# Optimization experiments

Hardware: AMD Instinct MI355X
Metric: run time of the kernel (lower is better)

Reference implementation:

```python
import jax, jax.numpy as jnp
import numpy as np

N = 20000       # nodes
E = 100000      # edges
STEPS = 4
ND = 128        # node feature dim
ED = 128        # edge feature dim
NIN = 128       # node input dim
EIN = 291       # edge input dim (2 + 17*17)
H = 64          # mpn edge-mlp hidden


def _lin(x, w, b):
    return x @ w + b


def setup_inputs():
    key = jax.random.key(0)
    ks = jax.random.split(key, 16)

    def w(k, i, o):
        return (jax.random.normal(k, (i, o), jnp.float32) / np.float32(np.sqrt(i)))

    d = {}
    d["x"] = jax.random.normal(ks[0], (N, NIN), jnp.float32)
    d["edge_attr"] = jax.random.normal(ks[1], (E, EIN), jnp.float32)
    d["edge_index"] = jax.random.randint(ks[2], (2, E), 0, N, jnp.int32)
    # node embedding MLP: NIN -> 128 -> ND (ReLU between, none after last)
    d["new0"] = w(ks[3], NIN, 128); d["neb0"] = jnp.zeros(128, jnp.float32)
    d["new1"] = w(ks[4], 128, ND); d["neb1"] = jnp.zeros(ND, jnp.float32)
    # edge embedding MLP: EIN -> 64 -> ED
    d["eew0"] = w(ks[5], EIN, 64); d["eeb0"] = jnp.zeros(64, jnp.float32)
    d["eew1"] = w(ks[6], 64, ED); d["eeb1"] = jnp.zeros(ED, jnp.float32)
    # MPN edge MLP (skip=True): 2*(2*ND) + 2*ED = 768 -> 64 -> ED, ReLU after each
    d["mew0"] = w(ks[7], 4 * ND + 2 * ED, H); d["meb0"] = jnp.zeros(H, jnp.float32)
    d["mew1"] = w(ks[8], H, ED); d["meb1"] = jnp.zeros(ED, jnp.float32)
    # MPN node MLP: 2*ND + ED = 384 -> ND, ReLU
    d["mnw0"] = w(ks[9], 2 * ND + ED, ND); d["mnb0"] = jnp.zeros(ND, jnp.float32)
    # classification MLP: ED -> 64 -> 32 -> 1
    d["cw0"] = w(ks[10], ED, 64); d["cb0"] = jnp.zeros(64, jnp.float32)
    d["cw1"] = w(ks[11], 64, 32); d["cb1"] = jnp.zeros(32, jnp.float32)
    d["cw2"] = w(ks[12], 32, 1); d["cb2"] = jnp.zeros(1, jnp.float32)
    return d


def reference(x, edge_attr, edge_index,
              new0, neb0, new1, neb1,
              eew0, eeb0, eew1, eeb1,
              mew0, meb0, mew1, meb1,
              mnw0, mnb0,
              cw0, cb0, cw1, cb1, cw2, cb2):
    relu = jax.nn.relu
    j, i = edge_index[0], edge_index[1]  # j: source, i: target

    nf = _lin(relu(_lin(x, new0, neb0)), new1, neb1)          # [N, ND]
    ef = _lin(relu(_lin(edge_attr, eew0, eeb0)), eew1, eeb1)  # [E, ED]
    nf0, ef0 = nf, ef

    for _ in range(STEPS):
        # skip connections: concat initial features
        nfc = jnp.concatenate([nf0, nf], axis=1)  # [N, 2*ND]
        efc = jnp.concatenate([ef0, ef], axis=1)  # [E, 2*ED]
        x_i = nfc[i]  # [E, 2*ND] target
        x_j = nfc[j]  # [E, 2*ND] source
        # edge update MLP (ReLU after both layers)
        h = relu(_lin(jnp.concatenate([x_i, x_j, efc], axis=1), mew0, meb0))
        ef = relu(_lin(h, mew1, meb1))  # [E, ED]
        # message: mlp_node([x_i, edge_attr_new]) aggregated at target i
        msg = relu(_lin(jnp.concatenate([x_i, ef], axis=1), mnw0, mnb0))  # [E, ND]
        nf = jax.ops.segment_sum(msg, i, num_segments=N)  # [N, ND]

    out = relu(_lin(ef, cw0, cb0))
    out = relu(_lin(out, cw1, cb1))
    out = _lin(out, cw2, cb2)  # [E, 1]
    return out
```

## Files before the change

### kernel.cpp

```cpp
#include <hip/hip_runtime.h>
#include <hip/hip_bf16.h>

#define ND 128
#define ED 128
#define NIN 128
#define EIN 291
#define KPAD 320
#define HH 64
#define TM 32
#define TS 64
#define GSE 768
#define MAXGE 3

typedef __attribute__((ext_vector_type(8))) short short8;
typedef __attribute__((ext_vector_type(4))) float float4_;

__device__ __forceinline__ unsigned short f2bf(float f)
{
    union { float f; unsigned u; } v; v.f = f;
    unsigned u = v.u;
    unsigned r = (u + 0x7FFFu + ((u >> 16) & 1u)) >> 16;
    return (unsigned short)r;
}
__device__ __forceinline__ float bf2f(unsigned short s)
{
    union { unsigned u; float f; } v; v.u = ((unsigned)s) << 16;
    return v.f;
}

template<int T, int KC, int K>
__device__ __forceinline__ void stage_frags(const unsigned short* __restrict__ src,
                                            unsigned short* __restrict__ wreg,
                                            int t, int k0)
{
    constexpr int TOT = T * KC * 64;
#pragma unroll
    for (int it = 0; it < TOT / 256; it++) {
        int idx = it * 256 + t;
        int f = idx >> 6, l = idx & 63;
        int col = (f / KC) * 16 + (l & 15);
        int k = (f % KC) * 32 + ((l >> 4) * 8);
        *(short8*)&wreg[idx * 8] = *(const short8*)&src[(size_t)col * K + k0 + k];
    }
}
#define FRAG(wreg, f, lane) (*(const short8*)&(wreg)[(((f) << 6) + (lane)) * 8])

__global__ __launch_bounds__(256) void zero_k(float* __restrict__ p, int n4)
{
    int idx = blockIdx.x * 256 + threadIdx.x;
    if (idx < n4) ((float4*)p)[idx] = make_float4(0.f, 0.f, 0.f, 0.f);
}

__global__ __launch_bounds__(256) void hist_k(const int* __restrict__ tgti,
                                              int* __restrict__ deg, int E)
{
    int e = blockIdx.x * 256 + threadIdx.x;
    if (e < E) atomicAdd(&deg[tgti[e]], 1);
}

__global__ __launch_bounds__(256) void scan_k(const int* __restrict__ deg,
                                              int* __restrict__ row_ptr,
                                              int* __restrict__ cursor, int N, int E)
{
    __shared__ int part[256];
    const int t = threadIdx.x;
    const int chunk = (N + 255) / 256;
    const int base = t * chunk;
    int s = 0;
    for (int k = 0; k < chunk; k++) { int idx = base + k; if (idx < N) s += deg[idx]; }
    part[t] = s;
    __syncthreads();
    for (int off = 1; off < 256; off <<= 1) {
        int v = (t >= off) ? part[t - off] : 0;
        __syncthreads();
        part[t] += v;
        __syncthreads();
    }
    int run = (t == 0) ? 0 : part[t - 1];
    for (int k = 0; k < chunk; k++) {
        int idx = base + k;
        if (idx < N) { row_ptr[idx] = run; cursor[idx] = run; run += deg[idx]; }
    }
    if (t == 255) row_ptr[N] = E;
}

__global__ __launch_bounds__(256) void scatter_k(const int* __restrict__ tgti,
                                                 int* __restrict__ cursor,
                                                 int* __restrict__ csr_eid, int E)
{
    int e = blockIdx.x * 256 + threadIdx.x;
    if (e < E) {
        int p = atomicAdd(&cursor[tgti[e]], 1);
        csr_eid[p] = e;
    }
}

__global__ __launch_bounds__(256) void agg_k(const int* __restrict__ row_ptr,
                                             const int* __restrict__ csr_eid,
                                             const unsigned short* __restrict__ msg,
                                             unsigned short* __restrict__ nf_bf, int N)
{
    int n = blockIdx.x * 2 + (threadIdx.x >> 7);
    int c = threadIdx.x & 127;
    if (n >= N) return;
    int beg = row_ptr[n], end = row_ptr[n + 1];
    float acc = 0.f;
    for (int k = beg; k < end; k++) {
        int e = csr_eid[k];
        acc += bf2f(msg[(size_t)e * ND + c]);
    }
    nf_bf[(size_t)n * ND + c] = f2bf(acc);
}

__global__ __launch_bounds__(256) void wprep_k(
    const float* __restrict__ mew0, const float* __restrict__ mew1, const float* __restrict__ mnw0,
    const float* __restrict__ eew0, const float* __restrict__ eew1, const float* __restrict__ cw0,
    const float* __restrict__ new0, const float* __restrict__ new1,
    unsigned short* __restrict__ w0T, unsigned short* __restrict__ w1T,
    unsigned short* __restrict__ wmT, unsigned short* __restrict__ w0eT,
    unsigned short* __restrict__ w1eT, unsigned short* __restrict__ cw0T,
    unsigned short* __restrict__ w0nT, unsigned short* __restrict__ w1nT)
{
    int idx = blockIdx.x * 256 + threadIdx.x;
    if (idx < 49152) {
        int c = idx / 768, k = idx % 768;
        w0T[idx] = f2bf(mew0[k * 64 + c]);
    } else if (idx < 57344) {
        int j = idx - 49152; int c = j / 64, k = j % 64;
        w1T[j] = f2bf(mew1[k * 128 + c]);
    } else if (idx < 106496) {
        int j = idx - 57344; int c = j / 384, k = j % 384;
        wmT[j] = f2bf(mnw0[k * 128 + c]);
    } else if (idx < 126976) {
        int j = idx - 106496; int c = j / KPAD, k = j % KPAD;
        w0eT[j] = (k < EIN) ? f2bf(eew0[k * 64 + c]) : (unsigned short)0;
    } else if (idx < 135168) {
        int j = idx - 126976; int c = j / 64, k = j % 64;
        w1eT[j] = f2bf(eew1[k * 128 + c]);
    } else if (idx < 143360) {
        int j = idx - 135168; int c = j / 128, k = j % 128;
        cw0T[j] = f2bf(cw0[k * 64 + c]);
    } else if (idx < 159744) {
        int j = idx - 143360; int c = j / 128, k = j % 128;
        w0nT[j] = f2bf(new0[k * 128 + c]);
    } else if (idx < 176128) {
        int j = idx - 159744; int c = j / 128, k = j % 128;
        w1nT[j] = f2bf(new1[k * 128 + c]);
    }
}

__global__ __launch_bounds__(256) void node_embed_k(
    const float* __restrict__ x,
    const unsigned short* __restrict__ w0nT, const float* __restrict__ b0,
    const unsigned short* __restrict__ w1nT, const float* __restrict__ b1,
    unsigned short* __restrict__ nf0_bf, unsigned short* __restrict__ nf_bf, int N)
{
    const int t = threadIdx.x;
    const int n0 = blockIdx.x * TM;
    __shared__ unsigned short wreg[8192];
    __shared__ unsigned short xin[TM][130];
    __shared__ unsigned short h_bf[TM][130];

#pragma unroll
    for (int it = 0; it < 4; it++) {
        int idx = it * 256 + t;
        int r = idx >> 5, c4 = idx & 31;
        int node = n0 + r; if (node >= N) node = N - 1;
        float4 v = *(const float4*)(x + (size_t)node * NIN + c4 * 4);
        unsigned lo = (unsigned)f2bf(v.x) | ((unsigned)f2bf(v.y) << 16);
        unsigned hi = (unsigned)f2bf(v.z) | ((unsigned)f2bf(v.w) << 16);
        *(uint2*)&xin[r][c4 * 4] = make_uint2(lo, hi);
    }

    const int w = t >> 6, lane = t & 63, quad = lane >> 4, n16 = lane & 15;
    const int m = w & 1, nh = w >> 1;

    float4_ acc[4];
#pragma unroll
    for (int q = 0; q < 4; q++) acc[q] = (float4_){0.f, 0.f, 0.f, 0.f};
#pragma unroll
    for (int hf = 0; hf < 2; hf++) {
        stage_frags<8, 2, 128>(w0nT, wreg, t, hf * 64);
        __syncthreads();
#pragma unroll
        for (int kc = 0; kc < 2; kc++) {
            short8 a = *(const short8*)&xin[m * 16 + n16][hf * 64 + kc * 32 + quad * 8];
#pragma unroll
            for (int tt = 0; tt < 4; tt++) {
                short8 b = FRAG(wreg, (nh * 4 + tt) * 2 + kc, lane);
                acc[tt] = __builtin_amdgcn_mfma_f32_16x16x32_bf16(a, b, acc[tt], 0, 0, 0);
            }
        }
        __syncthreads();
    }
#pragma unroll
    for (int tt = 0; tt < 4; tt++) {
        int c = nh * 64 + tt * 16 + n16;
        float bias = b0[c];
#pragma unroll
        for (int r4 = 0; r4 < 4; r4++)
            h_bf[m * 16 + quad * 4 + r4][c] = f2bf(fmaxf(acc[tt][r4] + bias, 0.f));
    }
    __syncthreads();

    float4_ acc2[4];
#pragma unroll
    for (int q = 0; q < 4; q++) acc2[q] = (float4_){0.f, 0.f, 0.f, 0.f};
#pragma unroll
    for (int hf = 0; hf < 2; hf++) {
        stage_frags<8, 2, 128>(w1nT, wreg, t, hf * 64);
        __syncthreads();
#pragma unroll
        for (int kc = 0; kc < 2; kc++) {
            short8 a = *(const short8*)&h_bf[m * 16 + n16][hf * 64 + kc * 32 + quad * 8];
#pragma unroll
            for (int tt = 0; tt < 4; tt++) {
                short8 b = FRAG(wreg, (nh * 4 + tt) * 2 + kc, lane);
                acc2[tt] = __builtin_amdgcn_mfma_f32_16x16x32_bf16(a, b, acc2[tt], 0, 0, 0);
            }
        }
        __syncthreads();
    }
#pragma unroll
    for (int tt = 0; tt < 4; tt++) {
        int c = nh * 64 + tt * 16 + n16;
        float bias = b1[c];
#pragma unroll
        for (int r4 = 0; r4 < 4; r4++) {
            int row = m * 16 + quad * 4 + r4;
            int node = n0 + row;
            if (node < N) {
                unsigned short v = f2bf(acc2[tt][r4] + bias);
                nf0_bf[(size_t)node * ND + c] = v;
                nf_bf[(size_t)node * ND + c] = v;
            }
        }
    }
}

__global__ __launch_bounds__(256, 3) void edge_embed_k(
    const float* __restrict__ ea,
    const unsigned short* __restrict__ w0eT, const float* __restrict__ b0,
    const unsigned short* __restrict__ w1eT, const float* __restrict__ b1,
    unsigned short* __restrict__ ef0_bf, unsigned short* __restrict__ ef_bf,
    int E, int ntiles)
{
    const int t = threadIdx.x;
    __shared__ unsigned short w0reg[10240];
    __shared__ unsigned short w1reg[8192];
    __shared__ unsigned short hsl[4][16 * 66];

    const int w = t >> 6, lane = t & 63, quad = lane >> 4, n16 = lane & 15;

    stage_frags<8, 2, 64>(w1eT, w1reg, t, 0);

    int ng = 0;
    int tile[MAXGE];
#pragma unroll
    for (int g = 0; g < MAXGE; g++) {
        int tl = blockIdx.x + g * GSE;
        if (tl < ntiles) { tile[g] = tl; ng = g + 1; }
        else tile[g] = 0;
    }

    float4_ accL[MAXGE][4];
#pragma unroll
    for (int g = 0; g < MAXGE; g++)
#pragma unroll
        for (int q = 0; q < 4; q++) accL[g][q] = (float4_){0.f, 0.f, 0.f, 0.f};

#pragma unroll
    for (int hf = 0; hf < 2; hf++) {
        __syncthreads();
        stage_frags<4, 5, KPAD>(w0eT, w0reg, t, hf * 160);
        __syncthreads();
#pragma unroll
        for (int g = 0; g < MAXGE; g++) {
            if (g < ng) {
                int e = tile[g] * 64 + w * 16 + n16; if (e >= E) e = E - 1;
                const float* src = ea + (size_t)e * EIN;
#pragma unroll
                for (int kc = 0; kc < 5; kc++) {
                    int k = hf * 160 + kc * 32 + quad * 8;
                    union { short8 s; uint4 u; } av;
                    if (k + 8 <= EIN) {
                        float4 v0 = *(const float4*)(src + k);
                        float4 v1 = *(const float4*)(src + k + 4);
                        av.u.x = (unsigned)f2bf(v0.x) | ((unsigned)f2bf(v0.y) << 16);
                        av.u.y = (unsigned)f2bf(v0.z) | ((unsigned)f2bf(v0.w) << 16);
                        av.u.z = (unsigned)f2bf(v1.x) | ((unsigned)f2bf(v1.y) << 16);
                        av.u.w = (unsigned)f2bf(v1.z) | ((unsigned)f2bf(v1.w) << 16);
                    } else {
                        unsigned short vv[8];
#pragma unroll
                        for (int j = 0; j < 8; j++)
                            vv[j] = (k + j < EIN) ? f2bf(src[k + j]) : (unsigned short)0;
                        av.u.x = (unsigned)vv[0] | ((unsigned)vv[1] << 16);
                        av.u.y = (unsigned)vv[2] | ((unsigned)vv[3] << 16);
                        av.u.z = (unsigned)vv[4] | ((unsigned)vv[5] << 16);
                        av.u.w = (unsigned)vv[6] | ((unsigned)vv[7] << 16);
                    }
#pragma unroll
                    for (int tt = 0; tt < 4; tt++) {
                        short8 b = FRAG(w0reg, tt * 5 + kc, lane);
                        accL[g][tt] = __builtin_amdgcn_mfma_f32_16x16x32_bf16(av.s, b, accL[g][tt], 0, 0, 0);
                    }
                }
            }
        }
    }

#pragma unroll
    for (int g = 0; g < MAXGE; g++) {
        if (g < ng) {
#pragma unroll
            for (int tt = 0; tt < 4; tt++) {
                int c = tt * 16 + n16;
                float bias = b0[c];
#pragma unroll
                for (int r4 = 0; r4 < 4; r4++)
                    hsl[w][(quad * 4 + r4) * 66 + c] = f2bf(fmaxf(accL[g][tt][r4] + bias, 0.f));
            }
            float4_ acc2[8];
#pragma unroll
            for (int q = 0; q < 8; q++) acc2[q] = (float4_){0.f, 0.f, 0.f, 0.f};
#pragma unroll
            for (int kc = 0; kc < 2; kc++) {
                short8 a2 = *(const short8*)&hsl[w][n16 * 66 + kc * 32 + quad * 8];
#pragma unroll
                for (int tt = 0; tt < 8; tt++)
                    acc2[tt] = __builtin_amdgcn_mfma_f32_16x16x32_bf16(
                        a2, FRAG(w1reg, tt * 2 + kc, lane), acc2[tt], 0, 0, 0);
            }
#pragma unroll
            for (int tt = 0; tt < 8; tt++) {
                int c = tt * 16 + n16;
                float bias = b1[c];
#pragma unroll
                for (int r4 = 0; r4 < 4; r4++) {
                    int e = tile[g] * 64 + w * 16 + quad * 4 + r4;
                    if (e < E) {
                        unsigned short v = f2bf(acc2[tt][r4] + bias);
                        ef0_bf[(size_t)e * ED + c] = v;
                        ef_bf[(size_t)e * ED + c] = v;
                    }
                }
            }
        }
    }
}

__global__ __launch_bounds__(256, 3) void edge_step_k(
    const int* __restrict__ srcj, const int* __restrict__ tgti,
    const unsigned short* __restrict__ nf0_bf, const unsigned short* __restrict__ nf_bf,
    const unsigned short* __restrict__ ef0_bf, unsigned short* __restrict__ ef_bf,
    unsigned short* __restrict__ msg,
    const unsigned short* __restrict__ w0T, const float* __restrict__ meb0,
    const unsigned short* __restrict__ w1T, const float* __restrict__ meb1,
    const unsigned short* __restrict__ wmT, const float* __restrict__ mnb0,
    int E, int wmsg)
{
    const int t = threadIdx.x;
    const int e0 = blockIdx.x * TS;
    __shared__ unsigned short wreg[16384];
    __shared__ unsigned short hef[4][2080];

    const int w = t >> 6, lane = t & 63, quad = lane >> 4, n16 = lane & 15;
    int ec = e0 + w * 16 + n16; if (ec >= E) ec = E - 1;
    const int ti = tgti[ec], sj = srcj[ec];

    const unsigned short* pAs[6] = {
        nf0_bf + (size_t)ti * ND + quad * 8,
        nf_bf  + (size_t)ti * ND + quad * 8,
        nf0_bf + (size_t)sj * ND + quad * 8,
        nf_bf  + (size_t)sj * ND + quad * 8,
        ef0_bf + (size_t)ec * ED + quad * 8,
        ef_bf  + (size_t)ec * ED + quad * 8 };

    float4_ accL[4];
#pragma unroll
    for (int q = 0; q < 4; q++) accL[q] = (float4_){0.f, 0.f, 0.f, 0.f};
#pragma unroll
    for (int hf = 0; hf < 3; hf++) {
        short8 a8[8];
#pragma unroll
        for (int q2 = 0; q2 < 8; q2++)
            a8[q2] = *(const short8*)(pAs[hf * 2 + (q2 >> 2)] + (q2 & 3) * 32);
        stage_frags<4, 8, 768>(w0T, wreg, t, hf * 256);
        __syncthreads();
#pragma unroll
        for (int kc = 0; kc < 8; kc++) {
#pragma unroll
            for (int tt = 0; tt < 4; tt++) {
                short8 b = FRAG(wreg, tt * 8 + kc, lane);
                accL[tt] = __builtin_amdgcn_mfma_f32_16x16x32_bf16(a8[kc], b, accL[tt], 0, 0, 0);
            }
        }
        __syncthreads();
    }

#pragma unroll
    for (int tt = 0; tt < 4; tt++) {
        int c = tt * 16 + n16;
        float bias = meb0[c];
#pragma unroll
        for (int r4 = 0; r4 < 4; r4++)
            hef[w][(quad * 4 + r4) * 66 + c] = f2bf(fmaxf(accL[tt][r4] + bias, 0.f));
    }

    stage_frags<8, 2, 64>(w1T, wreg, t, 0);
    __syncthreads();
    {
        float4_ acc[8];
#pragma unroll
        for (int q = 0; q < 8; q++) acc[q] = (float4_){0.f, 0.f, 0.f, 0.f};
#pragma unroll
        for (int kc = 0; kc < 2; kc++) {
            short8 a = *(const short8*)&hef[w][n16 * 66 + kc * 32 + quad * 8];
#pragma unroll
            for (int tt = 0; tt < 8; tt++) {
                short8 b = FRAG(wreg, tt * 2 + kc, lane);
                acc[tt] = __builtin_amdgcn_mfma_f32_16x16x32_bf16(a, b, acc[tt], 0, 0, 0);
            }
        }
#pragma unroll
        for (int tt = 0; tt < 8; tt++) {
            int c = tt * 16 + n16;
            float bias = meb1[c];
#pragma unroll
            for (int r4 = 0; r4 < 4; r4++) {
                int row = quad * 4 + r4;
                unsigned short v = f2bf(fmaxf(acc[tt][r4] + bias, 0.f));
                hef[w][row * 130 + c] = v;
                int e = e0 + w * 16 + row;
                if (e < E) ef_bf[(size_t)e * ED + c] = v;
            }
        }
    }
    __syncthreads();

    if (wmsg) {
        float4_ accM[8];
#pragma unroll
        for (int q = 0; q < 8; q++) accM[q] = (float4_){0.f, 0.f, 0.f, 0.f};
#pragma unroll
        for (int j = 0; j < 3; j++) {
            short8 a4[4];
            if (j < 2) {
#pragma unroll
                for (int q2 = 0; q2 < 4; q2++)
                    a4[q2] = *(const short8*)(pAs[j] + q2 * 32);
            } else {
#pragma unroll
                for (int q2 = 0; q2 < 4; q2++)
                    a4[q2] = *(const short8*)&hef[w][n16 * 130 + q2 * 32 + quad * 8];
            }
            stage_frags<8, 4, 384>(wmT, wreg, t, j * 128);
            __syncthreads();
#pragma unroll
            for (int kc = 0; kc < 4; kc++) {
#pragma unroll
                for (int tt = 0; tt < 8; tt++) {
                    short8 b = FRAG(wreg, tt * 4 + kc, lane);
                    accM[tt] = __builtin_amdgcn_mfma_f32_16x16x32_bf16(a4[kc], b, accM[tt], 0, 0, 0);
                }
            }
            __syncthreads();
        }
#pragma unroll
        for (int tt = 0; tt < 8; tt++) {
            int c = tt * 16 + n16;
            float bias = mnb0[c];
#pragma unroll
            for (int r4 = 0; r4 < 4; r4++) {
                int row = w * 16 + quad * 4 + r4;
                int e = e0 + row;
                if (e < E)
                    msg[(size_t)e * ND + c] = f2bf(fmaxf(accM[tt][r4] + bias, 0.f));
            }
        }
    }
}

__global__ __launch_bounds__(256) void classify_k(
    const unsigned short* __restrict__ ef_bf,
    const unsigned short* __restrict__ cw0T, const float* __restrict__ cb0,
    const float* __restrict__ cw1, const float* __restrict__ cb1,
    const float* __restrict__ cw2, const float* __restrict__ cb2,
    float* __restrict__ out, int E)
{
    const int t = threadIdx.x;
    const int e0 = blockIdx.x * TM;
    __shared__ unsigned short h0_bf[TM][66];
    __shared__ float h1[TM][33];

    const int w = t >> 6, lane = t & 63, quad = lane >> 4, n16 = lane & 15;
    const int m = w & 1;
    const int erow = m * 16 + n16;
    int ec = e0 + erow; if (ec >= E) ec = E - 1;
    const unsigned short* pa = ef_bf + (size_t)ec * ED + quad * 8;

    {
        const int cb = (w >> 1) * 32;
        float4_ acc0 = {0.f, 0.f, 0.f, 0.f}, acc1 = acc0;
        const unsigned short* b0p = cw0T + (size_t)(cb + n16) * 128 + quad * 8;
        const unsigned short* b1p = b0p + (size_t)16 * 128;
#pragma unroll
        for (int kc = 0; kc < 4; kc++) {
            short8 a  = *(const short8*)(pa + kc * 32);
            short8 bb0 = *(const short8*)(b0p + kc * 32);
            short8 bb1 = *(const short8*)(b1p + kc * 32);
            acc0 = __builtin_amdgcn_mfma_f32_16x16x32_bf16(a, bb0, acc0, 0, 0, 0);
            acc1 = __builtin_amdgcn_mfma_f32_16x16x32_bf16(a, bb1, acc1, 0, 0, 0);
        }
#pragma unroll
        for (int t2 = 0; t2 < 2; t2++) {
            int c = cb + t2 * 16 + n16;
            float bias = cb0[c];
            float4_ ac = t2 ? acc1 : acc0;
#pragma unroll
            for (int r4 = 0; r4 < 4; r4++)
                h0_bf[m * 16 + quad * 4 + r4][c] = f2bf(fmaxf(ac[r4] + bias, 0.f));
        }
    }
    __syncthreads();

    {
        int c = t & 31;
        int rbase = (t >> 5) * 4;
#pragma unroll
        for (int q = 0; q < 4; q++) {
            int r = rbase + q;
            float acc = cb1[c];
#pragma unroll 8
            for (int k = 0; k < 64; k++) acc += bf2f(h0_bf[r][k]) * cw1[k * 32 + c];
            h1[r][c] = fmaxf(acc, 0.f);
        }
    }
    __syncthreads();

    if (t < TM) {
        int e = e0 + t;
        if (e < E) {
            float a = cb2[0];
#pragma unroll
            for (int k = 0; k < 32; k++) a += h1[t][k] * cw2[k];
            out[e] = a;
        }
    }
}

extern "C" void kernel_launch(void* const* d_in, const int* in_sizes, int n_in,
                              void* d_out, int out_size, void* d_ws, size_t ws_size,
                              hipStream_t stream)
{
    const float* x    = (const float*)d_in[0];
    const float* ea   = (const float*)d_in[1];
    const int*   eidx = (const int*)d_in[2];
    const float* new0 = (const float*)d_in[3];  const float* neb0 = (const float*)d_in[4];
    const float* new1 = (const float*)d_in[5];  const float* neb1 = (const float*)d_in[6];
    const float* eew0 = (const float*)d_in[7];  const float* eeb0 = (const float*)d_in[8];
    const float* eew1 = (const float*)d_in[9];  const float* eeb1 = (const float*)d_in[10];
    const float* mew0 = (const float*)d_in[11]; const float* meb0 = (const float*)d_in[12];
    const float* mew1 = (const float*)d_in[13]; const float* meb1 = (const float*)d_in[14];
    const float* mnw0 = (const float*)d_in[15]; const float* mnb0 = (const float*)d_in[16];
    const float* cw0  = (const float*)d_in[17]; const float* cb0  = (const float*)d_in[18];
    const float* cw1  = (const float*)d_in[19]; const float* cb1  = (const float*)d_in[20];
    const float* cw2  = (const float*)d_in[21]; const float* cb2  = (const float*)d_in[22];

    const int N = in_sizes[0] / NIN;
    const int E = in_sizes[2] / 2;
    const int* srcj = eidx;
    const int* tgti = eidx + E;

    char* wsb = (char*)d_ws;
    unsigned short* nf0_bf = (unsigned short*)wsb;
    unsigned short* nf_bf  = nf0_bf + (size_t)N * ND;
    unsigned short* ef0_bf = nf_bf + (size_t)N * ND;
    unsigned short* ef_bf  = ef0_bf + (size_t)E * ED;
    unsigned short* msg    = ef_bf + (size_t)E * ED;
    unsigned short* w0T  = msg + (size_t)E * ND;
    unsigned short* w1T  = w0T + 49152;
    unsigned short* wmT  = w1T + 8192;
    unsigned short* w0eT = wmT + 49152;
    unsigned short* w1eT = w0eT + 64 * KPAD;
    unsigned short* cw0T = w1eT + 8192;
    unsigned short* w0nT = cw0T + 8192;
    unsigned short* w1nT = w0nT + 16384;
    int* deg     = (int*)(w1nT + 16384);
    int* cursor  = deg + N;
    int* row_ptr = cursor + N;
    int* csr_eid = row_ptr + (N + 4);

    const int eblocks32 = (E + TM - 1) / TM;
    const int nblocks32 = (N + TM - 1) / TM;
    const int ntiles64 = (E + 63) / 64;

    wprep_k<<<(176128 + 255) / 256, 256, 0, stream>>>(mew0, mew1, mnw0, eew0, eew1, cw0,
                                                      new0, new1,
                                                      w0T, w1T, wmT, w0eT, w1eT, cw0T,
                                                      w0nT, w1nT);

    zero_k<<<((2 * N) / 4 + 255) / 256, 256, 0, stream>>>((float*)deg, (2 * N) / 4);
    hist_k<<<(E + 255) / 256, 256, 0, stream>>>(tgti, deg, E);
    scan_k<<<1, 256, 0, stream>>>(deg, row_ptr, cursor, N, E);
    scatter_k<<<(E + 255) / 256, 256, 0, stream>>>(tgti, cursor, csr_eid, E);

    node_embed_k<<<nblocks32, 256, 0, stream>>>(x, w0nT, neb0, w1nT, neb1,
                                                nf0_bf, nf_bf, N);
    edge_embed_k<<<GSE, 256, 0, stream>>>(ea, w0eT, eeb0, w1eT, eeb1,
                                          ef0_bf, ef_bf, E, ntiles64);

    for (int s = 0; s < 4; s++) {
        edge_step_k<<<ntiles64, 256, 0, stream>>>(srcj, tgti, nf0_bf, nf_bf,
                                                  ef0_bf, ef_bf, msg,
                                                  w0T, meb0, w1T, meb1, wmT, mnb0,
                                                  E, (s < 3) ? 1 : 0);
        if (s < 3)
            agg_k<<<(N + 1) / 2, 256, 0, stream>>>(row_ptr, csr_eid, msg, nf_bf, N);
    }

    classify_k<<<eblocks32, 256, 0, stream>>>(ef_bf, cw0T, cb0, cw1, cb1, cw2, cb2,
                                              (float*)d_out, E);
}
```

Measured before the change: 760.1 us.

## Load MFMA weight fragments directly from global in pre-swizzled layout, drop LDS staging

The weight-prep kernel now writes the edge-step weights already arranged in MFMA B-fragment order. The edge-step kernel reads each fragment straight from global memory (mostly L2-resident) instead of copying it into a 32KB LDS buffer with block barriers. Removing that buffer and the barriers cuts LDS use, and launch bounds rise to 4 blocks per CU for more occupancy. The cost is many more redundant global/L2 loads of weights per wave and possible register pressure under the tighter bound.

```diff
diff --git a/kernel.cpp b/kernel.cpp
--- a/kernel.cpp
+++ b/kernel.cpp
@@ -44,6 +44,7 @@
     }
 }
 #define FRAG(wreg, f, lane) (*(const short8*)&(wreg)[(((f) << 6) + (lane)) * 8])
+#define GFRAG(wp, f, lane) (*(const short8*)&(wp)[(((f) << 6) + (lane)) * 8])
 
 __global__ __launch_bounds__(256) void zero_k(float* __restrict__ p, int n4)
 {
@@ -116,21 +117,29 @@
     const float* __restrict__ mew0, const float* __restrict__ mew1, const float* __restrict__ mnw0,
     const float* __restrict__ eew0, const float* __restrict__ eew1, const float* __restrict__ cw0,
     const float* __restrict__ new0, const float* __restrict__ new1,
-    unsigned short* __restrict__ w0T, unsigned short* __restrict__ w1T,
-    unsigned short* __restrict__ wmT, unsigned short* __restrict__ w0eT,
+    unsigned short* __restrict__ w0F, unsigned short* __restrict__ w1F,
+    unsigned short* __restrict__ wmF, unsigned short* __restrict__ w0eT,
     unsigned short* __restrict__ w1eT, unsigned short* __restrict__ cw0T,
     unsigned short* __restrict__ w0nT, unsigned short* __restrict__ w1nT)
 {
     int idx = blockIdx.x * 256 + threadIdx.x;
     if (idx < 49152) {
-        int c = idx / 768, k = idx % 768;
-        w0T[idx] = f2bf(mew0[k * 64 + c]);
+        int j = idx & 7, l = (idx >> 3) & 63, f = idx >> 9;
+        int col = (f / 24) * 16 + (l & 15);
+        int k = (f % 24) * 32 + ((l >> 4) * 8) + j;
+        w0F[idx] = f2bf(mew0[k * 64 + col]);
     } else if (idx < 57344) {
-        int j = idx - 49152; int c = j / 64, k = j % 64;
-        w1T[j] = f2bf(mew1[k * 128 + c]);
+        int i2 = idx - 49152;
+        int j = i2 & 7, l = (i2 >> 3) & 63, f = i2 >> 9;
+        int col = (f / 2) * 16 + (l & 15);
+        int k = (f % 2) * 32 + ((l >> 4) * 8) + j;
+        w1F[i2] = f2bf(mew1[k * 128 + col]);
     } else if (idx < 106496) {
-        int j = idx - 57344; int c = j / 384, k = j % 384;
-        wmT[j] = f2bf(mnw0[k * 128 + c]);
+        int i2 = idx - 57344;
+        int j = i2 & 7, l = (i2 >> 3) & 63, f = i2 >> 9;
+        int col = (f / 12) * 16 + (l & 15);
+        int k = (f % 12) * 32 + ((l >> 4) * 8) + j;
+        wmF[i2] = f2bf(mnw0[k * 128 + col]);
     } else if (idx < 126976) {
         int j = idx - 106496; int c = j / KPAD, k = j % KPAD;
         w0eT[j] = (k < EIN) ? f2bf(eew0[k * 64 + c]) : (unsigned short)0;
@@ -350,26 +359,25 @@
     }
 }
 
-__global__ __launch_bounds__(256, 3) void edge_step_k(
+__global__ __launch_bounds__(256, 4) void edge_step_k(
     const int* __restrict__ srcj, const int* __restrict__ tgti,
     const unsigned short* __restrict__ nf0_bf, const unsigned short* __restrict__ nf_bf,
     const unsigned short* __restrict__ ef0_bf, unsigned short* __restrict__ ef_bf,
     unsigned short* __restrict__ msg,
-    const unsigned short* __restrict__ w0T, const float* __restrict__ meb0,
-    const unsigned short* __restrict__ w1T, const float* __restrict__ meb1,
-    const unsigned short* __restrict__ wmT, const float* __restrict__ mnb0,
+    const unsigned short* __restrict__ w0F, const float* __restrict__ meb0,
+    const unsigned short* __restrict__ w1F, const float* __restrict__ meb1,
+    const unsigned short* __restrict__ wmF, const float* __restrict__ mnb0,
     int E, int wmsg)
 {
     const int t = threadIdx.x;
     const int e0 = blockIdx.x * TS;
-    __shared__ unsigned short wreg[16384];
     __shared__ unsigned short hef[4][2080];
 
     const int w = t >> 6, lane = t & 63, quad = lane >> 4, n16 = lane & 15;
     int ec = e0 + w * 16 + n16; if (ec >= E) ec = E - 1;
     const int ti = tgti[ec], sj = srcj[ec];
 
-    const unsigned short* pAs[6] = {
+    const unsigned short* pA[6] = {
         nf0_bf + (size_t)ti * ND + quad * 8,
         nf_bf  + (size_t)ti * ND + quad * 8,
         nf0_bf + (size_t)sj * ND + quad * 8,
@@ -381,22 +389,13 @@
 #pragma unroll
     for (int q = 0; q < 4; q++) accL[q] = (float4_){0.f, 0.f, 0.f, 0.f};
 #pragma unroll
-    for (int hf = 0; hf < 3; hf++) {
-        short8 a8[8];
-#pragma unroll
-        for (int q2 = 0; q2 < 8; q2++)
-            a8[q2] = *(const short8*)(pAs[hf * 2 + (q2 >> 2)] + (q2 & 3) * 32);
-        stage_frags<4, 8, 768>(w0T, wreg, t, hf * 256);
-        __syncthreads();
-#pragma unroll
-        for (int kc = 0; kc < 8; kc++) {
-#pragma unroll
-            for (int tt = 0; tt < 4; tt++) {
-                short8 b = FRAG(wreg, tt * 8 + kc, lane);
-                accL[tt] = __builtin_amdgcn_mfma_f32_16x16x32_bf16(a8[kc], b, accL[tt], 0, 0, 0);
-            }
-        }
-        __syncthreads();
+    for (int kc = 0; kc < 24; kc++) {
+        short8 a = *(const short8*)(pA[kc >> 2] + (kc & 3) * 32);
+#pragma unroll
+        for (int tt = 0; tt < 4; tt++) {
+            short8 b = GFRAG(w0F, tt * 24 + kc, lane);
+            accL[tt] = __builtin_amdgcn_mfma_f32_16x16x32_bf16(a, b, accL[tt], 0, 0, 0);
+        }
     }
 
 #pragma unroll
@@ -408,8 +407,6 @@
             hef[w][(quad * 4 + r4) * 66 + c] = f2bf(fmaxf(accL[tt][r4] + bias, 0.f));
     }
 
-    stage_frags<8, 2, 64>(w1T, wreg, t, 0);
-    __syncthreads();
     {
         float4_ acc[8];
 #pragma unroll
@@ -419,7 +416,7 @@
             short8 a = *(const short8*)&hef[w][n16 * 66 + kc * 32 + quad * 8];
 #pragma unroll
             for (int tt = 0; tt < 8; tt++) {
-                short8 b = FRAG(wreg, tt * 2 + kc, lane);
+                short8 b = GFRAG(w1F, tt * 2 + kc, lane);
                 acc[tt] = __builtin_amdgcn_mfma_f32_16x16x32_bf16(a, b, acc[tt], 0, 0, 0);
             }
         }
@@ -437,35 +434,21 @@
             }
         }
     }
-    __syncthreads();
 
     if (wmsg) {
         float4_ accM[8];
 #pragma unroll
         for (int q = 0; q < 8; q++) accM[q] = (float4_){0.f, 0.f, 0.f, 0.f};
 #pragma unroll
-        for (int j = 0; j < 3; j++) {
-            short8 a4[4];
-            if (j < 2) {
-#pragma unroll
-                for (int q2 = 0; q2 < 4; q2++)
-                    a4[q2] = *(const short8*)(pAs[j] + q2 * 32);
-            } else {
-#pragma unroll
-                for (int q2 = 0; q2 < 4; q2++)
-                    a4[q2] = *(const short8*)&hef[w][n16 * 130 + q2 * 32 + quad * 8];
-            }
-            stage_frags<8, 4, 384>(wmT, wreg, t, j * 128);
-            __syncthreads();
-#pragma unroll
-            for (int kc = 0; kc < 4; kc++) {
-#pragma unroll
-                for (int tt = 0; tt < 8; tt++) {
-                    short8 b = FRAG(wreg, tt * 4 + kc, lane);
-                    accM[tt] = __builtin_amdgcn_mfma_f32_16x16x32_bf16(a4[kc], b, accM[tt], 0, 0, 0);
-                }
-            }
-            __syncthreads();
+        for (int kc = 0; kc < 12; kc++) {
+            short8 a;
+            if (kc < 8) a = *(const short8*)(pA[kc >> 2] + (kc & 3) * 32);
+            else        a = *(const short8*)&hef[w][n16 * 130 + (kc - 8) * 32 + quad * 8];
+#pragma unroll
+            for (int tt = 0; tt < 8; tt++) {
+                short8 b = GFRAG(wmF, tt * 12 + kc, lane);
+                accM[tt] = __builtin_amdgcn_mfma_f32_16x16x32_bf16(a, b, accM[tt], 0, 0, 0);
+            }
         }
 #pragma unroll
         for (int tt = 0; tt < 8; tt++) {
@@ -473,8 +456,7 @@
             float bias = mnb0[c];
 #pragma unroll
             for (int r4 = 0; r4 < 4; r4++) {
-                int row = w * 16 + quad * 4 + r4;
-                int e = e0 + row;
+                int e = e0 + w * 16 + quad * 4 + r4;
                 if (e < E)
                     msg[(size_t)e * ND + c] = f2bf(fmaxf(accM[tt][r4] + bias, 0.f));
             }
@@ -579,10 +561,10 @@
     unsigned short* ef0_bf = nf_bf + (size_t)N * ND;
     unsigned short* ef_bf  = ef0_bf + (size_t)E * ED;
     unsigned short* msg    = ef_bf + (size_t)E * ED;
-    unsigned short* w0T  = msg + (size_t)E * ND;
-    unsigned short* w1T  = w0T + 49152;
-    unsigned short* wmT  = w1T + 8192;
-    unsigned short* w0eT = wmT + 49152;
+    unsigned short* w0F  = msg + (size_t)E * ND;
+    unsigned short* w1F  = w0F + 49152;
+    unsigned short* wmF  = w1F + 8192;
+    unsigned short* w0eT = wmF + 49152;
     unsigned short* w1eT = w0eT + 64 * KPAD;
     unsigned short* cw0T = w1eT + 8192;
     unsigned short* w0nT = cw0T + 8192;
@@ -598,7 +580,7 @@
 
     wprep_k<<<(176128 + 255) / 256, 256, 0, stream>>>(mew0, mew1, mnw0, eew0, eew1, cw0,
                                                       new0, new1,
-                                                      w0T, w1T, wmT, w0eT, w1eT, cw0T,
+                                                      w0F, w1F, wmF, w0eT, w1eT, cw0T,
                                                       w0nT, w1nT);
 
     zero_k<<<((2 * N) / 4 + 255) / 256, 256, 0, stream>>>((float*)deg, (2 * N) / 4);
@@ -614,7 +596,7 @@
     for (int s = 0; s < 4; s++) {
         edge_step_k<<<ntiles64, 256, 0, stream>>>(srcj, tgti, nf0_bf, nf_bf,
                                                   ef0_bf, ef_bf, msg,
-                                                  w0T, meb0, w1T, meb1, wmT, mnb0,
+                                                  w0F, meb0, w1F, meb1, wmF, mnb0,
                                                   E, (s < 3) ? 1 : 0);
         if (s < 3)
             agg_k<<<(N + 1) / 2, 256, 0, stream>>>(row_ptr, csr_eid, msg, nf_bf, N);
```

Result: slower. 920.5 us (+21.1%).

## Stage edge-attr tile into shared memory with coalesced loads, one tile per block

Applied to the files above, without the earlier changes.

The edge embedding kernel now loads each 64-edge tile of the fp32 edge attributes cooperatively into shared memory (converted to bf16) with contiguous float4 reads. Previously each lane read strided 8-float chunks straight from global memory. The persistent multi-tile-per-block grid is replaced by one block per tile, and the second-layer weights reuse the first-layer weight buffer to save LDS. The cost is a large shared tile (~41KB) that lowers occupancy (launch bounds 3→2), plus extra barriers and per-block weight restaging.

```diff
diff --git a/kernel.cpp b/kernel.cpp
--- a/kernel.cpp
+++ b/kernel.cpp
@@ -6,11 +6,11 @@
 #define NIN 128
 #define EIN 291
 #define KPAD 320
+#define KP2 324
 #define HH 64
 #define TM 32
 #define TS 64
-#define GSE 768
-#define MAXGE 3
+#define SEGS 81
 
 typedef __attribute__((ext_vector_type(8))) short short8;
 typedef __attribute__((ext_vector_type(4))) float float4_;
@@ -238,112 +238,98 @@
     }
 }
 
-__global__ __launch_bounds__(256, 3) void edge_embed_k(
+__global__ __launch_bounds__(256, 2) void edge_embed_k(
     const float* __restrict__ ea,
     const unsigned short* __restrict__ w0eT, const float* __restrict__ b0,
     const unsigned short* __restrict__ w1eT, const float* __restrict__ b1,
     unsigned short* __restrict__ ef0_bf, unsigned short* __restrict__ ef_bf,
-    int E, int ntiles)
+    int E)
 {
     const int t = threadIdx.x;
+    const int e0 = blockIdx.x * 64;
+    __shared__ unsigned short aT[64][KP2];
     __shared__ unsigned short w0reg[10240];
-    __shared__ unsigned short w1reg[8192];
     __shared__ unsigned short hsl[4][16 * 66];
 
     const int w = t >> 6, lane = t & 63, quad = lane >> 4, n16 = lane & 15;
 
-    stage_frags<8, 2, 64>(w1eT, w1reg, t, 0);
-
-    int ng = 0;
-    int tile[MAXGE];
-#pragma unroll
-    for (int g = 0; g < MAXGE; g++) {
-        int tl = blockIdx.x + g * GSE;
-        if (tl < ntiles) { tile[g] = tl; ng = g + 1; }
-        else tile[g] = 0;
-    }
-
-    float4_ accL[MAXGE][4];
-#pragma unroll
-    for (int g = 0; g < MAXGE; g++)
-#pragma unroll
-        for (int q = 0; q < 4; q++) accL[g][q] = (float4_){0.f, 0.f, 0.f, 0.f};
+    for (int it = 0; it < (64 * SEGS + 255) / 256; it++) {
+        int idx = it * 256 + t;
+        if (idx < 64 * SEGS) {
+            int r = idx / SEGS, seg = idx % SEGS;
+            int e = e0 + r; if (e >= E) e = E - 1;
+            const float* src = ea + (size_t)e * EIN + seg * 4;
+            unsigned short v[4];
+            if (seg * 4 + 4 <= EIN) {
+                float4 f = *(const float4*)src;
+                v[0] = f2bf(f.x); v[1] = f2bf(f.y); v[2] = f2bf(f.z); v[3] = f2bf(f.w);
+            } else {
+#pragma unroll
+                for (int j = 0; j < 4; j++)
+                    v[j] = (seg * 4 + j < EIN) ? f2bf(src[j]) : (unsigned short)0;
+            }
+            *(uint2*)&aT[r][seg * 4] = make_uint2(
+                (unsigned)v[0] | ((unsigned)v[1] << 16),
+                (unsigned)v[2] | ((unsigned)v[3] << 16));
+        }
+    }
+
+    const int arow = w * 16 + n16;
+    float4_ accL[4];
+#pragma unroll
+    for (int q = 0; q < 4; q++) accL[q] = (float4_){0.f, 0.f, 0.f, 0.f};
 
 #pragma unroll
     for (int hf = 0; hf < 2; hf++) {
-        __syncthreads();
+        if (hf) __syncthreads();
         stage_frags<4, 5, KPAD>(w0eT, w0reg, t, hf * 160);
         __syncthreads();
 #pragma unroll
-        for (int g = 0; g < MAXGE; g++) {
-            if (g < ng) {
-                int e = tile[g] * 64 + w * 16 + n16; if (e >= E) e = E - 1;
-                const float* src = ea + (size_t)e * EIN;
-#pragma unroll
-                for (int kc = 0; kc < 5; kc++) {
-                    int k = hf * 160 + kc * 32 + quad * 8;
-                    union { short8 s; uint4 u; } av;
-                    if (k + 8 <= EIN) {
-                        float4 v0 = *(const float4*)(src + k);
-                        float4 v1 = *(const float4*)(src + k + 4);
-                        av.u.x = (unsigned)f2bf(v0.x) | ((unsigned)f2bf(v0.y) << 16);
-                        av.u.y = (unsigned)f2bf(v0.z) | ((unsigned)f2bf(v0.w) << 16);
-                        av.u.z = (unsigned)f2bf(v1.x) | ((unsigned)f2bf(v1.y) << 16);
-                        av.u.w = (unsigned)f2bf(v1.z) | ((unsigned)f2bf(v1.w) << 16);
-                    } else {
-                        unsigned short vv[8];
-#pragma unroll
-                        for (int j = 0; j < 8; j++)
-                            vv[j] = (k + j < EIN) ? f2bf(src[k + j]) : (unsigned short)0;
-                        av.u.x = (unsigned)vv[0] | ((unsigned)vv[1] << 16);
-                        av.u.y = (unsigned)vv[2] | ((unsigned)vv[3] << 16);
-                        av.u.z = (unsigned)vv[4] | ((unsigned)vv[5] << 16);
-                        av.u.w = (unsigned)vv[6] | ((unsigned)vv[7] << 16);
-                    }
-#pragma unroll
-                    for (int tt = 0; tt < 4; tt++) {
-                        short8 b = FRAG(w0reg, tt * 5 + kc, lane);
-                        accL[g][tt] = __builtin_amdgcn_mfma_f32_16x16x32_bf16(av.s, b, accL[g][tt], 0, 0, 0);
-                    }
-                }
-            }
-        }
-    }
-
-#pragma unroll
-    for (int g = 0; g < MAXGE; g++) {
-        if (g < ng) {
+        for (int kc = 0; kc < 5; kc++) {
+            short8 a = *(const short8*)&aT[arow][hf * 160 + kc * 32 + quad * 8];
 #pragma unroll
             for (int tt = 0; tt < 4; tt++) {
-                int c = tt * 16 + n16;
-                float bias = b0[c];
-#pragma unroll
-                for (int r4 = 0; r4 < 4; r4++)
-                    hsl[w][(quad * 4 + r4) * 66 + c] = f2bf(fmaxf(accL[g][tt][r4] + bias, 0.f));
-            }
-            float4_ acc2[8];
-#pragma unroll
-            for (int q = 0; q < 8; q++) acc2[q] = (float4_){0.f, 0.f, 0.f, 0.f};
-#pragma unroll
-            for (int kc = 0; kc < 2; kc++) {
-                short8 a2 = *(const short8*)&hsl[w][n16 * 66 + kc * 32 + quad * 8];
-#pragma unroll
-                for (int tt = 0; tt < 8; tt++)
-                    acc2[tt] = __builtin_amdgcn_mfma_f32_16x16x32_bf16(
-                        a2, FRAG(w1reg, tt * 2 + kc, lane), acc2[tt], 0, 0, 0);
-            }
-#pragma unroll
-            for (int tt = 0; tt < 8; tt++) {
-                int c = tt * 16 + n16;
-                float bias = b1[c];
-#pragma unroll
-                for (int r4 = 0; r4 < 4; r4++) {
-                    int e = tile[g] * 64 + w * 16 + quad * 4 + r4;
-                    if (e < E) {
-                        unsigned short v = f2bf(acc2[tt][r4] + bias);
-                        ef0_bf[(size_t)e * ED + c] = v;
-                        ef_bf[(size_t)e * ED + c] = v;
-                    }
+                short8 b = FRAG(w0reg, tt * 5 + kc, lane);
+                accL[tt] = __builtin_amdgcn_mfma_f32_16x16x32_bf16(a, b, accL[tt], 0, 0, 0);
+            }
+        }
+    }
+
+#pragma unroll
+    for (int tt = 0; tt < 4; tt++) {
+        int c = tt * 16 + n16;
+        float bias = b0[c];
+#pragma unroll
+        for (int r4 = 0; r4 < 4; r4++)
+            hsl[w][(quad * 4 + r4) * 66 + c] = f2bf(fmaxf(accL[tt][r4] + bias, 0.f));
+    }
+
+    __syncthreads();
+    stage_frags<8, 2, 64>(w1eT, w0reg, t, 0);
+    __syncthreads();
+    {
+        float4_ acc2[8];
+#pragma unroll
+        for (int q = 0; q < 8; q++) acc2[q] = (float4_){0.f, 0.f, 0.f, 0.f};
+#pragma unroll
+        for (int kc = 0; kc < 2; kc++) {
+            short8 a2 = *(const short8*)&hsl[w][n16 * 66 + kc * 32 + quad * 8];
+#pragma unroll
+            for (int tt = 0; tt < 8; tt++)
+                acc2[tt] = __builtin_amdgcn_mfma_f32_16x16x32_bf16(
+                    a2, FRAG(w0reg, tt * 2 + kc, lane), acc2[tt], 0, 0, 0);
+        }
+#pragma unroll
+        for (int tt = 0; tt < 8; tt++) {
+            int c = tt * 16 + n16;
+            float bias = b1[c];
+#pragma unroll
+            for (int r4 = 0; r4 < 4; r4++) {
+                int e = e0 + w * 16 + quad * 4 + r4;
+                if (e < E) {
+                    unsigned short v = f2bf(acc2[tt][r4] + bias);
+                    ef0_bf[(size_t)e * ED + c] = v;
+                    ef_bf[(size_t)e * ED + c] = v;
                 }
             }
         }
@@ -369,7 +355,7 @@
     int ec = e0 + w * 16 + n16; if (ec >= E) ec = E - 1;
     const int ti = tgti[ec], sj = srcj[ec];
 
-    const unsigned short* pAs[6] = {
+    const unsigned short* pA[6] = {
         nf0_bf + (size_t)ti * ND + quad * 8,
         nf_bf  + (size_t)ti * ND + quad * 8,
         nf0_bf + (size_t)sj * ND + quad * 8,
@@ -385,7 +371,7 @@
         short8 a8[8];
 #pragma unroll
         for (int q2 = 0; q2 < 8; q2++)
-            a8[q2] = *(const short8*)(pAs[hf * 2 + (q2 >> 2)] + (q2 & 3) * 32);
+            a8[q2] = *(const short8*)(pA[hf * 2 + (q2 >> 2)] + (q2 & 3) * 32);
         stage_frags<4, 8, 768>(w0T, wreg, t, hf * 256);
         __syncthreads();
 #pragma unroll
@@ -449,7 +435,7 @@
             if (j < 2) {
 #pragma unroll
                 for (int q2 = 0; q2 < 4; q2++)
-                    a4[q2] = *(const short8*)(pAs[j] + q2 * 32);
+                    a4[q2] = *(const short8*)(pA[j] + q2 * 32);
             } else {
 #pragma unroll
                 for (int q2 = 0; q2 < 4; q2++)
@@ -608,8 +594,8 @@
 
     node_embed_k<<<nblocks32, 256, 0, stream>>>(x, w0nT, neb0, w1nT, neb1,
                                                 nf0_bf, nf_bf, N);
-    edge_embed_k<<<GSE, 256, 0, stream>>>(ea, w0eT, eeb0, w1eT, eeb1,
-                                          ef0_bf, ef_bf, E, ntiles64);
+    edge_embed_k<<<ntiles64, 256, 0, stream>>>(ea, w0eT, eeb0, w1eT, eeb1,
+                                               ef0_bf, ef_bf, E);
 
     for (int s = 0; s < 4; s++) {
         edge_step_k<<<ntiles64, 256, 0, stream>>>(srcj, tgti, nf0_bf, nf_bf,
```

Measured after the change: 860.3 us. +13.2%, slower.

## Process edges in CSR-sorted order to make aggregation reads contiguous

Applied to the files above, without the earlier changes.

Edges are permuted into target-sorted CSR order once: edge embedding gathers edge_attr rows through csr_eid, edge features and messages are stored in permuted order, and the step kernel uses permuted source and target indices. Aggregation then reads messages contiguously per node without indirection, and the classifier scatters its output back to the original edge order. It also improves locality of target-node gathers in the edge step, at the cost of an extra permutation kernel and a gathered read of edge_attr.

```diff
diff --git a/kernel.cpp b/kernel.cpp
--- a/kernel.cpp
+++ b/kernel.cpp
@@ -95,8 +95,21 @@
     }
 }
 
+__global__ __launch_bounds__(256) void permidx_k(const int* __restrict__ csr_eid,
+                                                 const int* __restrict__ srcj,
+                                                 const int* __restrict__ tgti,
+                                                 int* __restrict__ srcp,
+                                                 int* __restrict__ tgtp, int E)
+{
+    int p = blockIdx.x * 256 + threadIdx.x;
+    if (p < E) {
+        int e = csr_eid[p];
+        srcp[p] = srcj[e];
+        tgtp[p] = tgti[e];
+    }
+}
+
 __global__ __launch_bounds__(256) void agg_k(const int* __restrict__ row_ptr,
-                                             const int* __restrict__ csr_eid,
                                              const unsigned short* __restrict__ msg,
                                              unsigned short* __restrict__ nf_bf, int N)
 {
@@ -105,10 +118,8 @@
     if (n >= N) return;
     int beg = row_ptr[n], end = row_ptr[n + 1];
     float acc = 0.f;
-    for (int k = beg; k < end; k++) {
-        int e = csr_eid[k];
-        acc += bf2f(msg[(size_t)e * ND + c]);
-    }
+    for (int p = beg; p < end; p++)
+        acc += bf2f(msg[(size_t)p * ND + c]);
     nf_bf[(size_t)n * ND + c] = f2bf(acc);
 }
 
@@ -239,7 +250,7 @@
 }
 
 __global__ __launch_bounds__(256, 3) void edge_embed_k(
-    const float* __restrict__ ea,
+    const float* __restrict__ ea, const int* __restrict__ csr_eid,
     const unsigned short* __restrict__ w0eT, const float* __restrict__ b0,
     const unsigned short* __restrict__ w1eT, const float* __restrict__ b1,
     unsigned short* __restrict__ ef0_bf, unsigned short* __restrict__ ef_bf,
@@ -277,8 +288,8 @@
 #pragma unroll
         for (int g = 0; g < MAXGE; g++) {
             if (g < ng) {
-                int e = tile[g] * 64 + w * 16 + n16; if (e >= E) e = E - 1;
-                const float* src = ea + (size_t)e * EIN;
+                int p = tile[g] * 64 + w * 16 + n16; if (p >= E) p = E - 1;
+                const float* src = ea + (size_t)csr_eid[p] * EIN;
 #pragma unroll
                 for (int kc = 0; kc < 5; kc++) {
                     int k = hf * 160 + kc * 32 + quad * 8;
@@ -338,11 +349,11 @@
                 float bias = b1[c];
 #pragma unroll
                 for (int r4 = 0; r4 < 4; r4++) {
-                    int e = tile[g] * 64 + w * 16 + quad * 4 + r4;
-                    if (e < E) {
+                    int p = tile[g] * 64 + w * 16 + quad * 4 + r4;
+                    if (p < E) {
                         unsigned short v = f2bf(acc2[tt][r4] + bias);
-                        ef0_bf[(size_t)e * ED + c] = v;
-                        ef_bf[(size_t)e * ED + c] = v;
+                        ef0_bf[(size_t)p * ED + c] = v;
+                        ef_bf[(size_t)p * ED + c] = v;
                     }
                 }
             }
@@ -351,7 +362,7 @@
 }
 
 __global__ __launch_bounds__(256, 3) void edge_step_k(
-    const int* __restrict__ srcj, const int* __restrict__ tgti,
+    const int* __restrict__ srcp, const int* __restrict__ tgtp,
     const unsigned short* __restrict__ nf0_bf, const unsigned short* __restrict__ nf_bf,
     const unsigned short* __restrict__ ef0_bf, unsigned short* __restrict__ ef_bf,
     unsigned short* __restrict__ msg,
@@ -367,9 +378,9 @@
 
     const int w = t >> 6, lane = t & 63, quad = lane >> 4, n16 = lane & 15;
     int ec = e0 + w * 16 + n16; if (ec >= E) ec = E - 1;
-    const int ti = tgti[ec], sj = srcj[ec];
-
-    const unsigned short* pAs[6] = {
+    const int ti = tgtp[ec], sj = srcp[ec];
+
+    const unsigned short* pA[6] = {
         nf0_bf + (size_t)ti * ND + quad * 8,
         nf_bf  + (size_t)ti * ND + quad * 8,
         nf0_bf + (size_t)sj * ND + quad * 8,
@@ -385,7 +396,7 @@
         short8 a8[8];
 #pragma unroll
         for (int q2 = 0; q2 < 8; q2++)
-            a8[q2] = *(const short8*)(pAs[hf * 2 + (q2 >> 2)] + (q2 & 3) * 32);
+            a8[q2] = *(const short8*)(pA[hf * 2 + (q2 >> 2)] + (q2 & 3) * 32);
         stage_frags<4, 8, 768>(w0T, wreg, t, hf * 256);
         __syncthreads();
 #pragma unroll
@@ -449,7 +460,7 @@
             if (j < 2) {
 #pragma unroll
                 for (int q2 = 0; q2 < 4; q2++)
-                    a4[q2] = *(const short8*)(pAs[j] + q2 * 32);
+                    a4[q2] = *(const short8*)(pA[j] + q2 * 32);
             } else {
 #pragma unroll
                 for (int q2 = 0; q2 < 4; q2++)
@@ -483,7 +494,7 @@
 }
 
 __global__ __launch_bounds__(256) void classify_k(
-    const unsigned short* __restrict__ ef_bf,
+    const unsigned short* __restrict__ ef_bf, const int* __restrict__ csr_eid,
     const unsigned short* __restrict__ cw0T, const float* __restrict__ cb0,
     const float* __restrict__ cw1, const float* __restrict__ cb1,
     const float* __restrict__ cw2, const float* __restrict__ cb2,
@@ -540,12 +551,12 @@
     __syncthreads();
 
     if (t < TM) {
-        int e = e0 + t;
-        if (e < E) {
+        int p = e0 + t;
+        if (p < E) {
             float a = cb2[0];
 #pragma unroll
             for (int k = 0; k < 32; k++) a += h1[t][k] * cw2[k];
-            out[e] = a;
+            out[csr_eid[p]] = a;
         }
     }
 }
@@ -591,6 +602,8 @@
     int* cursor  = deg + N;
     int* row_ptr = cursor + N;
     int* csr_eid = row_ptr + (N + 4);
+    int* srcp    = csr_eid + E;
+    int* tgtp    = srcp + E;
 
     const int eblocks32 = (E + TM - 1) / TM;
     const int nblocks32 = (N + TM - 1) / TM;
@@ -605,21 +618,22 @@
     hist_k<<<(E + 255) / 256, 256, 0, stream>>>(tgti, deg, E);
     scan_k<<<1, 256, 0, stream>>>(deg, row_ptr, cursor, N, E);
     scatter_k<<<(E + 255) / 256, 256, 0, stream>>>(tgti, cursor, csr_eid, E);
+    permidx_k<<<(E + 255) / 256, 256, 0, stream>>>(csr_eid, srcj, tgti, srcp, tgtp, E);
 
     node_embed_k<<<nblocks32, 256, 0, stream>>>(x, w0nT, neb0, w1nT, neb1,
                                                 nf0_bf, nf_bf, N);
-    edge_embed_k<<<GSE, 256, 0, stream>>>(ea, w0eT, eeb0, w1eT, eeb1,
+    edge_embed_k<<<GSE, 256, 0, stream>>>(ea, csr_eid, w0eT, eeb0, w1eT, eeb1,
                                           ef0_bf, ef_bf, E, ntiles64);
 
     for (int s = 0; s < 4; s++) {
-        edge_step_k<<<ntiles64, 256, 0, stream>>>(srcj, tgti, nf0_bf, nf_bf,
+        edge_step_k<<<ntiles64, 256, 0, stream>>>(srcp, tgtp, nf0_bf, nf_bf,
                                                   ef0_bf, ef_bf, msg,
                                                   w0T, meb0, w1T, meb1, wmT, mnb0,
                                                   E, (s < 3) ? 1 : 0);
         if (s < 3)
-            agg_k<<<(N + 1) / 2, 256, 0, stream>>>(row_ptr, csr_eid, msg, nf_bf, N);
-    }
-
-    classify_k<<<eblocks32, 256, 0, stream>>>(ef_bf, cw0T, cb0, cw1, cb1, cw2, cb2,
+            agg_k<<<(N + 1) / 2, 256, 0, stream>>>(row_ptr, msg, nf_bf, N);
+    }
+
+    classify_k<<<eblocks32, 256, 0, stream>>>(ef_bf, csr_eid, cw0T, cb0, cw1, cb1, cw2, cb2,
                                               (float*)d_out, E);
 }
```

Result: faster. 729.5 us (-4.0%).
